# Performance work log

Measured on AMD Instinct MI355X. Metric: run time of the kernel, lower is better.

## Reference

```python
import jax, jax.numpy as jnp
import numpy as np

# Model constants (match init_kwargs)
IN_DIM = 1024   # input_dim == OLA frame size
ST_DIM = 128    # state_dim
HOP = IN_DIM // 2
N_FRAMES = 512
N_SAMPLES = 262144  # n_frames * hop
CTX = 512       # context_dim == control_plane_dim
HD = 32         # hypernetwork_dim
HL = 16         # hypernetwork_latent
B = 8


def _make_w(hv, A, Bm, i, o):
    # HyperNetworkLayer: hypervector -> latent -> flattened (i, o) matrix per batch
    return (hv @ A @ Bm).reshape(-1, i, o)


def setup_inputs() -> dict:
    key = jax.random.key(0)
    ks = jax.random.split(key, 17)
    s = 0.05
    return {
        'control_signal': jax.random.normal(ks[0], (B, CTX, N_FRAMES), jnp.float32),
        'state_hv': jax.random.normal(ks[1], (B, HD), jnp.float32),
        'output_hv': jax.random.normal(ks[2], (B, HD), jnp.float32),
        'input_hv': jax.random.normal(ks[3], (B, HD), jnp.float32),
        'direct_hv': jax.random.normal(ks[4], (B, HD), jnp.float32),
        'proj_hv': jax.random.normal(ks[5], (B, HD), jnp.float32),
        'times': jax.random.normal(ks[6], (B, 1, N_FRAMES), jnp.float32),
        # hypernetwork parameters (learned)
        'A_proj': jax.random.normal(ks[7], (HD, HL), jnp.float32) * s,
        'B_proj': jax.random.normal(ks[8], (HL, CTX * IN_DIM), jnp.float32) * s,
        'A_state': jax.random.normal(ks[9], (HD, HL), jnp.float32) * s,
        'B_state': jax.random.normal(ks[10], (HL, ST_DIM * ST_DIM), jnp.float32) * s,
        'A_input': jax.random.normal(ks[11], (HD, HL), jnp.float32) * s,
        'B_input': jax.random.normal(ks[12], (HL, IN_DIM * ST_DIM), jnp.float32) * s,
        'A_output': jax.random.normal(ks[13], (HD, HL), jnp.float32) * s,
        'B_output': jax.random.normal(ks[14], (HL, ST_DIM * IN_DIM), jnp.float32) * s,
        'A_direct': jax.random.normal(ks[15], (HD, HL), jnp.float32) * s,
        'B_direct': jax.random.normal(ks[16], (HL, IN_DIM * IN_DIM), jnp.float32) * s,
    }


def _forward(control_signal, state_hv, output_hv, input_hv, direct_hv, proj_hv, times,
             A_proj, B_proj, A_state, B_state, A_input, B_input,
             A_output, B_output, A_direct, B_direct):
    batch = control_signal.shape[0]
    dt = control_signal.dtype
    # per-batch hypernetwork-generated dense matrices
    Wp = _make_w(proj_hv, A_proj, B_proj, CTX, IN_DIM)       # [b, ctx, in]
    Ws = _make_w(state_hv, A_state, B_state, ST_DIM, ST_DIM)  # [b, st, st]
    Wi = _make_w(input_hv, A_input, B_input, IN_DIM, ST_DIM)  # [b, in, st]
    Wo = _make_w(output_hv, A_output, B_output, ST_DIM, IN_DIM)
    Wd = _make_w(direct_hv, A_direct, B_direct, IN_DIM, IN_DIM)

    ctrl = jnp.transpose(control_signal ** 2, (0, 2, 1))       # [b, fr, ctx]
    proj = jnp.einsum('bfc,bci->bfi', ctrl, Wp)                # [b, fr, in]

    def step(s, u):
        # s_i = A s_{i-1} + B u_i ; y_i = C (A s_{i-1}) + D u_i
        s2 = jnp.einsum('bs,bst->bt', s, Ws)
        y = jnp.einsum('bt,bti->bi', s2, Wo) + jnp.einsum('bi,bij->bj', u, Wd)
        s_new = s2 + jnp.einsum('bi,bis->bs', u, Wi)
        return s_new, y

    s0 = jnp.zeros((batch, ST_DIM), dt)
    _, outs = jax.lax.scan(step, s0, jnp.transpose(proj, (1, 0, 2)))  # [fr, b, in]
    outs = jnp.transpose(outs, (1, 0, 2))                              # [b, fr, in]

    # overlap-add with periodic hann window, hop = in_dim // 2
    win = 0.5 - 0.5 * jnp.cos(2.0 * jnp.pi * jnp.arange(IN_DIM, dtype=dt) / IN_DIM)
    windowed = outs * win
    total = HOP * (N_FRAMES - 1) + IN_DIM
    idx = jnp.arange(N_FRAMES)[:, None] * HOP + jnp.arange(IN_DIM)[None, :]  # [fr, in]
    buf = jnp.zeros((batch, total), dt).at[:, idx].add(windowed)
    sig = buf[:, :N_SAMPLES][:, None, :]   # [b, 1, n_samples]

    # DiracScheduler.schedule: softmax impulses over frames, upsample, FFT convolve
    impulses = jax.nn.softmax(times, axis=-1)                  # [b, 1, fr]
    up = jnp.zeros((batch, 1, N_SAMPLES), dt).at[:, :, ::N_SAMPLES // N_FRAMES].set(impulses)
    n = 2 * N_SAMPLES
    y = jnp.fft.irfft(jnp.fft.rfft(sig, n=n) * jnp.fft.rfft(up, n=n), n=n)[..., :N_SAMPLES]
    return y.astype(dt)


def reference(control_signal, state_hv, output_hv, input_hv, direct_hv, proj_hv, times,
              A_proj, B_proj, A_state, B_state, A_input, B_input,
              A_output, B_output, A_direct, B_direct):
    return _forward(control_signal, state_hv, output_hv, input_hv, direct_hv, proj_hv, times,
                    A_proj, B_proj, A_state, B_state, A_input, B_input,
                    A_output, B_output, A_direct, B_direct)
```

## Files before the change

kernel.cpp:

```cpp
#include <hip/hip_runtime.h>
#include <math.h>


typedef __attribute__((ext_vector_type(8))) short bfrag;
typedef __attribute__((ext_vector_type(4))) float f32x4;

__device__ inline unsigned short f2bf(float f) {
  unsigned int u = __float_as_uint(f);
  unsigned int r = (u + 0x7fff + ((u >> 16) & 1)) >> 16;
  return (unsigned short)r;
}

static const size_t OFF_LAT   = 0;
static const size_t OFF_IMP   = 1024;
static const size_t OFF_WPT   = 139264;
static const size_t OFF_WOT   = 2236416;
static const size_t OFF_WDIT  = 2760704;
static const size_t OFF_CTRLT = 7479296;
static const size_t OFF_PROJ  = 8527872;
static const size_t OFF_PROJD = 10625024;
static const size_t OFF_S2    = 15343616;
static const size_t OFF_MPOW  = 15605760;
static const size_t OFF_EC    = 16785408;
static const size_t OFF_HC    = 16850944;
static const size_t OFF_Y     = 16916480;
static const size_t OFF_SIG   = 21110784;
static const size_t OFF_T     = 23207936;

__global__ void latents_kernel(
    const float* __restrict__ hv_p, const float* __restrict__ hv_s,
    const float* __restrict__ hv_i, const float* __restrict__ hv_o,
    const float* __restrict__ hv_d,
    const float* __restrict__ A_p, const float* __restrict__ A_s,
    const float* __restrict__ A_i, const float* __restrict__ A_o,
    const float* __restrict__ A_d,
    float* __restrict__ lat) {
  int tid = threadIdx.x;
  if (tid >= 640) return;
  int m = tid >> 7, b = (tid >> 4) & 7, l = tid & 15;
  const float* hv; const float* A;
  switch (m) {
    case 0: hv = hv_p; A = A_p; break;
    case 1: hv = hv_s; A = A_s; break;
    case 2: hv = hv_i; A = A_i; break;
    case 3: hv = hv_o; A = A_o; break;
    default: hv = hv_d; A = A_d; break;
  }
  float acc = 0.f;
  for (int h = 0; h < 32; ++h) acc = fmaf(hv[b * 32 + h], A[h * 16 + l], acc);
  lat[tid] = acc;
}

__global__ __launch_bounds__(256) void build_w_kernel(
    const float* __restrict__ lat,
    const float* __restrict__ Bm,
    float* __restrict__ out,
    int total, size_t bstride) {
  int e = (blockIdx.x * 256 + threadIdx.x) * 4;
  if (e >= total) return;
  float4 v[16];
#pragma unroll
  for (int l = 0; l < 16; ++l)
    v[l] = *(const float4*)(Bm + (size_t)l * total + e);
#pragma unroll 1
  for (int b = 0; b < 8; ++b) {
    float ax = 0.f, ay = 0.f, az = 0.f, aw = 0.f;
#pragma unroll
    for (int l = 0; l < 16; ++l) {
      float lv = lat[b * 16 + l];
      ax = fmaf(lv, v[l].x, ax);
      ay = fmaf(lv, v[l].y, ay);
      az = fmaf(lv, v[l].z, az);
      aw = fmaf(lv, v[l].w, aw);
    }
    *(float4*)(out + (size_t)b * bstride + e) = make_float4(ax, ay, az, aw);
  }
}

__global__ __launch_bounds__(256) void build_wt_kernel(
    const float* __restrict__ lat,
    const float* __restrict__ Bm,
    unsigned short* __restrict__ out,
    int R, int C, size_t bstride) {
  __shared__ float ls[128];
  __shared__ unsigned short tile[32][36];
  int tid = threadIdx.x;
  if (tid < 128) ls[tid] = lat[tid];
  int cc = tid & 31, rg = tid >> 5;
  int c = blockIdx.x * 32 + cc;
  int r0 = blockIdx.y * 32 + rg * 4;
  size_t RC = (size_t)R * C;
  float bm[16][4];
#pragma unroll
  for (int l = 0; l < 16; ++l) {
    const float* p = Bm + (size_t)l * RC + (size_t)r0 * C + c;
#pragma unroll
    for (int j = 0; j < 4; ++j) bm[l][j] = p[(size_t)j * C];
  }
  int wc = tid >> 3, wrq = tid & 7;
  __syncthreads();
#pragma unroll 1
  for (int b = 0; b < 8; ++b) {
    float a0 = 0.f, a1 = 0.f, a2 = 0.f, a3 = 0.f;
#pragma unroll
    for (int l = 0; l < 16; ++l) {
      float lv = ls[b * 16 + l];
      a0 = fmaf(lv, bm[l][0], a0);
      a1 = fmaf(lv, bm[l][1], a1);
      a2 = fmaf(lv, bm[l][2], a2);
      a3 = fmaf(lv, bm[l][3], a3);
    }
    __syncthreads();
    ushort2 p0, p1;
    p0.x = f2bf(a0); p0.y = f2bf(a1);
    p1.x = f2bf(a2); p1.y = f2bf(a3);
    *(ushort2*)&tile[cc][rg * 4] = p0;
    *(ushort2*)&tile[cc][rg * 4 + 2] = p1;
    __syncthreads();
    ushort4 v = *(const ushort4*)&tile[wc][wrq * 4];
    *(ushort4*)(out + (size_t)b * bstride +
                (size_t)(blockIdx.x * 32 + wc) * R + blockIdx.y * 32 + wrq * 4) = v;
  }
}

__global__ void transpose_sq_kernel(const float* __restrict__ in,
                                    unsigned short* __restrict__ out) {
  __shared__ float tile[32][33];
  int b = blockIdx.z;
  int c0 = blockIdx.x * 32, f0 = blockIdx.y * 32;
  int tx = threadIdx.x, ty = threadIdx.y;
  const float* inb = in + (size_t)b * 512 * 512;
  unsigned short* outb = out + (size_t)b * 512 * 512;
#pragma unroll
  for (int i = 0; i < 4; ++i) {
    float v = inb[(size_t)(c0 + ty + i * 8) * 512 + f0 + tx];
    tile[ty + i * 8][tx] = v * v;
  }
  __syncthreads();
#pragma unroll
  for (int i = 0; i < 4; ++i)
    outb[(size_t)(f0 + ty + i * 8) * 512 + c0 + tx] = f2bf(tile[tx][ty + i * 8]);
}

template <int EPI, int CD_BF16, int TRI>
__global__ __launch_bounds__(256) void mfma_gemm_kernel(
    const unsigned short* __restrict__ A,
    const unsigned short* __restrict__ BT,
    const float* __restrict__ D, int ldd,
    void* __restrict__ Cout,
    int M, int N, int K) {
  const int b = blockIdx.z;
  A  += (size_t)b * M * K;
  BT += (size_t)b * N * K;
  const int m0 = blockIdx.y * 128;
  const int n0 = blockIdx.x * 128;
  __shared__ __align__(16) unsigned short As[2][128][40];
  __shared__ __align__(16) unsigned short Bs[2][128][40];
  const int tid = threadIdx.x;
  const int lane = tid & 63, wave = tid >> 6;
  const int wr = (wave >> 1) * 64, wc = (wave & 1) * 64;
  const int l15 = lane & 15, g = lane >> 4;
  f32x4 acc[4][4];
#pragma unroll
  for (int i = 0; i < 4; ++i)
#pragma unroll
    for (int j = 0; j < 4; ++j)
#pragma unroll
      for (int r = 0; r < 4; ++r) acc[i][j][r] = 0.f;

  const int srow = tid >> 2, soct = tid & 3;
  const unsigned short* Ag = A + (size_t)(m0 + srow) * K + soct * 8;
  const unsigned short* Bg = BT + (size_t)(n0 + srow) * K + soct * 8;
  const size_t row64 = (size_t)64 * K;
  const int kend = TRI ? (m0 + 128) : K;
  const int nt = kend >> 5;

  bfrag av0 = *(const bfrag*)(Ag);
  bfrag av1 = *(const bfrag*)(Ag + row64);
  bfrag bv0 = *(const bfrag*)(Bg);
  bfrag bv1 = *(const bfrag*)(Bg + row64);

  int cur = 0;
#pragma unroll 1
  for (int t = 0; t < nt; ++t) {
    *(bfrag*)(&As[cur][srow][soct * 8]) = av0;
    *(bfrag*)(&As[cur][64 + srow][soct * 8]) = av1;
    *(bfrag*)(&Bs[cur][srow][soct * 8]) = bv0;
    *(bfrag*)(&Bs[cur][64 + srow][soct * 8]) = bv1;
    __syncthreads();
    if (t + 1 < nt) {
      const int k0 = (t + 1) << 5;
      av0 = *(const bfrag*)(Ag + k0);
      av1 = *(const bfrag*)(Ag + row64 + k0);
      bv0 = *(const bfrag*)(Bg + k0);
      bv1 = *(const bfrag*)(Bg + row64 + k0);
    }
    bfrag af[4], bf[4];
#pragma unroll
    for (int mi = 0; mi < 4; ++mi)
      af[mi] = *(const bfrag*)(&As[cur][wr + mi * 16 + l15][g * 8]);
#pragma unroll
    for (int nj = 0; nj < 4; ++nj)
      bf[nj] = *(const bfrag*)(&Bs[cur][wc + nj * 16 + l15][g * 8]);
#pragma unroll
    for (int mi = 0; mi < 4; ++mi)
#pragma unroll
      for (int nj = 0; nj < 4; ++nj)
        acc[mi][nj] = __builtin_amdgcn_mfma_f32_16x16x32_bf16(af[mi], bf[nj], acc[mi][nj], 0, 0, 0);
    cur ^= 1;
  }

  float* Cf = (float*)Cout + (size_t)b * M * N;
  unsigned short* Cb = (unsigned short*)Cout + (size_t)b * M * N;
  if (EPI) D += (size_t)b * M * ldd;
#pragma unroll
  for (int nj = 0; nj < 4; ++nj) {
    int n = n0 + wc + nj * 16 + l15;
    float win = 0.f;
    if (EPI) win = 0.5f - 0.5f * cosf(6.28318530717958647693f * (float)n / 1024.0f);
#pragma unroll
    for (int mi = 0; mi < 4; ++mi) {
      int mbase = m0 + wr + mi * 16 + 4 * g;
#pragma unroll
      for (int r = 0; r < 4; ++r) {
        int m = mbase + r;
        float v = acc[mi][nj][r];
        if (EPI) v = (v + D[(size_t)m * ldd + n]) * win;
        if (CD_BF16) Cb[(size_t)m * N + n] = f2bf(v);
        else         Cf[(size_t)m * N + n] = v;
      }
    }
  }
}

__global__ __launch_bounds__(256) void powers_kernel(float* __restrict__ Mpow, int half) {
  int z = blockIdx.x;
  int b = z / half, k = z - b * half + 1;
  const float* A = Mpow + ((size_t)b * 9 + k) * 16384;
  const float* Bm = Mpow + ((size_t)b * 9 + half) * 16384;
  float* C = Mpow + ((size_t)b * 9 + half + k) * 16384;
  __shared__ __align__(16) float As[16][132];
  __shared__ __align__(16) float Bs[16][132];
  int tid = threadIdx.x;
  int tx = tid & 15, ty = tid >> 4;
  float acc[8][8];
#pragma unroll
  for (int i = 0; i < 8; ++i)
#pragma unroll
    for (int j = 0; j < 8; ++j) acc[i][j] = 0.f;
  int ar = tid >> 1, ac = (tid & 1) * 8;
  int br = tid >> 4, bc = (tid & 15) * 8;
  for (int k0 = 0; k0 < 128; k0 += 16) {
    float4 a0 = *(const float4*)(A + (size_t)ar * 128 + k0 + ac);
    float4 a1 = *(const float4*)(A + (size_t)ar * 128 + k0 + ac + 4);
    float4 b0 = *(const float4*)(Bm + (size_t)(k0 + br) * 128 + bc);
    float4 b1 = *(const float4*)(Bm + (size_t)(k0 + br) * 128 + bc + 4);
    __syncthreads();
    As[ac + 0][ar] = a0.x; As[ac + 1][ar] = a0.y; As[ac + 2][ar] = a0.z; As[ac + 3][ar] = a0.w;
    As[ac + 4][ar] = a1.x; As[ac + 5][ar] = a1.y; As[ac + 6][ar] = a1.z; As[ac + 7][ar] = a1.w;
    *(float4*)(&Bs[br][bc]) = b0;
    *(float4*)(&Bs[br][bc + 4]) = b1;
    __syncthreads();
#pragma unroll
    for (int kk = 0; kk < 16; ++kk) {
      float4 av0 = *(const float4*)(&As[kk][ty * 8]);
      float4 av1 = *(const float4*)(&As[kk][ty * 8 + 4]);
      float4 bv0 = *(const float4*)(&Bs[kk][tx * 8]);
      float4 bv1 = *(const float4*)(&Bs[kk][tx * 8 + 4]);
      float aa[8] = {av0.x, av0.y, av0.z, av0.w, av1.x, av1.y, av1.z, av1.w};
      float bb[8] = {bv0.x, bv0.y, bv0.z, bv0.w, bv1.x, bv1.y, bv1.z, bv1.w};
#pragma unroll
      for (int i = 0; i < 8; ++i)
#pragma unroll
        for (int j = 0; j < 8; ++j) acc[i][j] = fmaf(aa[i], bb[j], acc[i][j]);
    }
  }
#pragma unroll
  for (int i = 0; i < 8; ++i) {
    *(float4*)(C + (size_t)(ty * 8 + i) * 128 + tx * 8) =
        make_float4(acc[i][0], acc[i][1], acc[i][2], acc[i][3]);
    *(float4*)(C + (size_t)(ty * 8 + i) * 128 + tx * 8 + 4) =
        make_float4(acc[i][4], acc[i][5], acc[i][6], acc[i][7]);
  }
}

__global__ __launch_bounds__(256) void ec_kernel(
    const float* __restrict__ Mpow, const float* __restrict__ PD,
    float* __restrict__ Ec) {
  int b = blockIdx.x >> 6, c = blockIdx.x & 63;
  int tid = threadIdx.x, t = tid & 127, dh = tid >> 7;
  __shared__ __align__(16) float Bus[7][128];
  __shared__ float red[128];
  const float* Bu = PD + (size_t)b * 512 * 1152 + 1024;
  for (int idx = tid; idx < 896; idx += 256)
    Bus[idx >> 7][idx & 127] = Bu[(size_t)(c * 8 + (idx >> 7)) * 1152 + (idx & 127)];
  __syncthreads();
  float acc = 0.f;
  const float* Mb = Mpow + (size_t)b * 9 * 16384;
  int d0 = dh * 64;
#pragma unroll
  for (int i = 0; i < 7; ++i) {
    const float* Mk = Mb + (size_t)(7 - i) * 16384 + t;
#pragma unroll 8
    for (int d = 0; d < 64; ++d)
      acc = fmaf(Bus[i][d0 + d], Mk[(size_t)(d0 + d) * 128], acc);
  }
  if (dh == 1) red[t] = acc;
  __syncthreads();
  if (dh == 0) {
    float tot = acc + red[t] + Bu[(size_t)(c * 8 + 7) * 1152 + t];
    Ec[((size_t)b * 64 + c) * 128 + t] = tot;
  }
}

__global__ __launch_bounds__(128) void combine_kernel(
    const float* __restrict__ Mpow, const float* __restrict__ Ec,
    float* __restrict__ Hc) {
  int b = blockIdx.x, t = threadIdx.x;
  float w[128];
  const float* M8 = Mpow + ((size_t)b * 9 + 8) * 16384;
#pragma unroll
  for (int k = 0; k < 128; ++k) w[k] = M8[(size_t)k * 128 + t];
  __shared__ __align__(16) float ec_sh[64 * 128];
  const float* Ecb = Ec + (size_t)b * 8192;
#pragma unroll
  for (int i = 0; i < 16; ++i) {
    int idx = (t + i * 128) * 4;
    *(float4*)&ec_sh[idx] = *(const float4*)(Ecb + idx);
  }
  __shared__ __align__(16) float sh[2][128];
  sh[0][t] = 0.f;
  float* Hcb = Hc + (size_t)b * 8192;
  Hcb[t] = 0.f;
  __syncthreads();
  int cur = 0;
#pragma unroll 1
  for (int c = 0; c < 63; ++c) {
    float a0 = 0.f, a1 = 0.f, a2 = 0.f, a3 = 0.f;
#pragma unroll
    for (int k = 0; k < 128; k += 4) {
      float4 sv = *(const float4*)(&sh[cur][k]);
      a0 = fmaf(sv.x, w[k + 0], a0);
      a1 = fmaf(sv.y, w[k + 1], a1);
      a2 = fmaf(sv.z, w[k + 2], a2);
      a3 = fmaf(sv.w, w[k + 3], a3);
    }
    float hn = (a0 + a1) + (a2 + a3) + ec_sh[c * 128 + t];
    sh[cur ^ 1][t] = hn;
    Hcb[(c + 1) * 128 + t] = hn;
    __syncthreads();
    cur ^= 1;
  }
}

__global__ __launch_bounds__(256) void pass2_kernel(
    const float* __restrict__ Mpow, const float* __restrict__ PD,
    const float* __restrict__ Hc, unsigned short* __restrict__ S2) {
  int b = blockIdx.x >> 6, c = blockIdx.x & 63;
  int tid = threadIdx.x, t = tid & 127, dh = tid >> 7;
  __shared__ __align__(16) float Xs[15][128];
  __shared__ __align__(16) float red[8][128];
  const float* Bu = PD + (size_t)b * 512 * 1152 + 1024;
  for (int idx = tid; idx < 15 * 128; idx += 256) {
    int rr = idx >> 7, cc = idx & 127;
    float v = 0.f;
    if (rr == 7) v = Hc[((size_t)b * 64 + c) * 128 + cc];
    else if (rr > 7) v = Bu[(size_t)(c * 8 + rr - 8) * 1152 + cc];
    Xs[rr][cc] = v;
  }
  __syncthreads();
  float acc[8];
#pragma unroll
  for (int j = 0; j < 8; ++j) acc[j] = 0.f;
  const float* Mb = Mpow + (size_t)b * 9 * 16384;
  int d0 = dh * 64;
#pragma unroll 1
  for (int k = 1; k <= 8; ++k) {
    const float* Mk = Mb + (size_t)k * 16384 + t;
    const int xbase = 8 - k;
#pragma unroll 4
    for (int d4 = 0; d4 < 16; ++d4) {
      int d = d0 + d4 * 4;
      float m0 = Mk[(size_t)(d + 0) * 128];
      float m1 = Mk[(size_t)(d + 1) * 128];
      float m2 = Mk[(size_t)(d + 2) * 128];
      float m3 = Mk[(size_t)(d + 3) * 128];
#pragma unroll
      for (int j = 0; j < 8; ++j) {
        float4 xv = *(const float4*)(&Xs[xbase + j][d]);
        acc[j] = fmaf(xv.x, m0, acc[j]);
        acc[j] = fmaf(xv.y, m1, acc[j]);
        acc[j] = fmaf(xv.z, m2, acc[j]);
        acc[j] = fmaf(xv.w, m3, acc[j]);
      }
    }
  }
  if (dh == 1) {
#pragma unroll
    for (int j = 0; j < 8; ++j) red[j][t] = acc[j];
  }
  __syncthreads();
  if (dh == 0) {
    unsigned short* S2b = S2 + ((size_t)b * 512 + c * 8) * 128;
#pragma unroll
    for (int j = 0; j < 8; ++j)
      S2b[(size_t)j * 128 + t] = f2bf(acc[j] + red[j][t]);
  }
}

__global__ void softmax_kernel(const float* __restrict__ times, float* __restrict__ imp) {
  int b = blockIdx.x, t = threadIdx.x;
  __shared__ float red[512];
  float v = times[b * 512 + t];
  red[t] = v;
  __syncthreads();
  for (int s = 256; s > 0; s >>= 1) {
    if (t < s) red[t] = fmaxf(red[t], red[t + s]);
    __syncthreads();
  }
  float m = red[0];
  __syncthreads();
  float e = expf(v - m);
  red[t] = e;
  __syncthreads();
  for (int s = 256; s > 0; s >>= 1) {
    if (t < s) red[t] += red[t + s];
    __syncthreads();
  }
  imp[b * 512 + t] = e / red[0];
}

__global__ void toeplitz_kernel(const float* __restrict__ imp, unsigned short* __restrict__ T) {
  int idx = blockIdx.x * 256 + threadIdx.x;
  int b = idx >> 16;
  int rem = idx & 65535;
  int q = rem >> 7, p4 = (rem & 127) * 4;
  const float* impb = imp + b * 512;
  ushort4 o;
  o.x = (p4 + 0 <= q) ? f2bf(impb[q - p4 - 0]) : (unsigned short)0;
  o.y = (p4 + 1 <= q) ? f2bf(impb[q - p4 - 1]) : (unsigned short)0;
  o.z = (p4 + 2 <= q) ? f2bf(impb[q - p4 - 2]) : (unsigned short)0;
  o.w = (p4 + 3 <= q) ? f2bf(impb[q - p4 - 3]) : (unsigned short)0;
  *(ushort4*)(T + ((size_t)b * 512 + q) * 512 + p4) = o;
}

__global__ __launch_bounds__(256) void ola_transpose_kernel(const float* __restrict__ Y,
                                                            unsigned short* __restrict__ sigT) {
  __shared__ unsigned short tile[64][72];
  int b = blockIdx.z;
  int q0 = blockIdx.x * 64, r0 = blockIdx.y * 64;
  int tid = threadIdx.x;
  int rr = tid & 63, qg = tid >> 6;
  const float* Yb = Y + (size_t)b * 512 * 1024;
#pragma unroll
  for (int i = 0; i < 16; ++i) {
    int q = q0 + qg * 16 + i;
    float v = Yb[(size_t)q * 1024 + r0 + rr];
    if (q > 0) v += Yb[(size_t)(q - 1) * 1024 + 512 + r0 + rr];
    tile[qg * 16 + i][rr] = f2bf(v);
  }
  __syncthreads();
  int rw = tid >> 2, qo = tid & 3;
  unsigned short* orow = sigT + ((size_t)b * 512 + r0 + rw) * 512 + q0 + qo * 16;
  ushort4 w0, w1, w2, w3;
  w0.x = tile[qo * 16 + 0][rw];  w0.y = tile[qo * 16 + 1][rw];
  w0.z = tile[qo * 16 + 2][rw];  w0.w = tile[qo * 16 + 3][rw];
  w1.x = tile[qo * 16 + 4][rw];  w1.y = tile[qo * 16 + 5][rw];
  w1.z = tile[qo * 16 + 6][rw];  w1.w = tile[qo * 16 + 7][rw];
  w2.x = tile[qo * 16 + 8][rw];  w2.y = tile[qo * 16 + 9][rw];
  w2.z = tile[qo * 16 + 10][rw]; w2.w = tile[qo * 16 + 11][rw];
  w3.x = tile[qo * 16 + 12][rw]; w3.y = tile[qo * 16 + 13][rw];
  w3.z = tile[qo * 16 + 14][rw]; w3.w = tile[qo * 16 + 15][rw];
  *(ushort4*)(orow + 0)  = w0;
  *(ushort4*)(orow + 4)  = w1;
  *(ushort4*)(orow + 8)  = w2;
  *(ushort4*)(orow + 12) = w3;
}

extern "C" void kernel_launch(void* const* d_in, const int* in_sizes, int n_in,
                              void* d_out, int out_size, void* d_ws, size_t ws_size,
                              hipStream_t stream) {
  const float* control   = (const float*)d_in[0];
  const float* state_hv  = (const float*)d_in[1];
  const float* output_hv = (const float*)d_in[2];
  const float* input_hv  = (const float*)d_in[3];
  const float* direct_hv = (const float*)d_in[4];
  const float* proj_hv   = (const float*)d_in[5];
  const float* times     = (const float*)d_in[6];
  const float* A_proj   = (const float*)d_in[7];
  const float* B_proj   = (const float*)d_in[8];
  const float* A_state  = (const float*)d_in[9];
  const float* B_state  = (const float*)d_in[10];
  const float* A_input  = (const float*)d_in[11];
  const float* B_input  = (const float*)d_in[12];
  const float* A_output = (const float*)d_in[13];
  const float* B_output = (const float*)d_in[14];
  const float* A_direct = (const float*)d_in[15];
  const float* B_direct = (const float*)d_in[16];

  float* ws = (float*)d_ws;
  float* lat  = ws + OFF_LAT;
  float* impw = ws + OFF_IMP;
  unsigned short* WpT   = (unsigned short*)(ws + OFF_WPT);
  unsigned short* WoT   = (unsigned short*)(ws + OFF_WOT);
  unsigned short* WdiT  = (unsigned short*)(ws + OFF_WDIT);
  unsigned short* ctrlT = (unsigned short*)(ws + OFF_CTRLT);
  unsigned short* proj  = (unsigned short*)(ws + OFF_PROJ);
  float* projD = ws + OFF_PROJD;
  unsigned short* S2 = (unsigned short*)(ws + OFF_S2);
  float* Mpow = ws + OFF_MPOW;
  float* Ec   = ws + OFF_EC;
  float* Hc   = ws + OFF_HC;
  float* Y    = ws + OFF_Y;
  unsigned short* sigT = (unsigned short*)(ws + OFF_SIG);
  unsigned short* Tb   = (unsigned short*)(ws + OFF_T);
  float* out  = (float*)d_out;

  latents_kernel<<<1, 640, 0, stream>>>(proj_hv, state_hv, input_hv, output_hv, direct_hv,
                                        A_proj, A_state, A_input, A_output, A_direct, lat);

  build_w_kernel<<<16, 256, 0, stream>>>(lat + 1 * 128, B_state, Mpow + 16384, 16384, 147456);

  build_wt_kernel<<<dim3(32, 16), 256, 0, stream>>>(lat + 0 * 128, B_proj, WpT, 512, 1024, 524288);
  build_wt_kernel<<<dim3(32, 32), 256, 0, stream>>>(lat + 4 * 128, B_direct, WdiT, 1024, 1024, 1179648);
  build_wt_kernel<<<dim3(4, 32), 256, 0, stream>>>(lat + 2 * 128, B_input, WdiT + 1024 * 1024, 1024, 128, 1179648);
  build_wt_kernel<<<dim3(32, 4), 256, 0, stream>>>(lat + 3 * 128, B_output, WoT, 128, 1024, 131072);

  transpose_sq_kernel<<<dim3(16, 16, 8), dim3(32, 8), 0, stream>>>(control, ctrlT);

  mfma_gemm_kernel<0, 1, 0><<<dim3(8, 4, 8), 256, 0, stream>>>(
      ctrlT, WpT, nullptr, 0, proj, 512, 1024, 512);

  mfma_gemm_kernel<0, 0, 0><<<dim3(9, 4, 8), 256, 0, stream>>>(
      proj, WdiT, nullptr, 0, projD, 512, 1152, 1024);

  powers_kernel<<<8, 256, 0, stream>>>(Mpow, 1);
  powers_kernel<<<16, 256, 0, stream>>>(Mpow, 2);
  powers_kernel<<<32, 256, 0, stream>>>(Mpow, 4);
  ec_kernel<<<512, 256, 0, stream>>>(Mpow, projD, Ec);
  combine_kernel<<<8, 128, 0, stream>>>(Mpow, Ec, Hc);
  pass2_kernel<<<512, 256, 0, stream>>>(Mpow, projD, Hc, S2);

  mfma_gemm_kernel<1, 0, 0><<<dim3(8, 4, 8), 256, 0, stream>>>(
      S2, WoT, projD, 1152, Y, 512, 1024, 128);

  softmax_kernel<<<8, 512, 0, stream>>>(times, impw);
  toeplitz_kernel<<<2048, 256, 0, stream>>>(impw, Tb);

  ola_transpose_kernel<<<dim3(8, 8, 8), 256, 0, stream>>>(Y, sigT);

  mfma_gemm_kernel<0, 0, 1><<<dim3(4, 4, 8), 256, 0, stream>>>(
      Tb, sigT, nullptr, 0, out, 512, 512, 512);
}
```

Before: 272.4 us.

## Merge weight-build kernels, fuse softmax/Toeplitz into conv GEMM, emit transposed bf16 Y

Replaces the latents, build_w, four build_wt and transpose launches with one megabuild kernel that computes latents per block and dispatches by block index. The softmax and Toeplitz construction are folded into a dedicated convolution MFMA kernel that builds the A tiles from shared-memory impulses, so the Toeplitz matrix is never written to global memory. The output GEMM now writes Y transposed in bf16, which lets a simple elementwise OLA kernel replace the shared-memory transpose. This cuts launch count and global traffic. In exchange, the softmax is recomputed in every conv block, the latent computation is repeated in every build block, and the intermediate Y is kept at lower precision.

Result: faster. 240.2 us (-11.8%).

```diff
diff --git a/kernel.cpp b/kernel.cpp
--- a/kernel.cpp
+++ b/kernel.cpp
@@ -10,8 +10,10 @@
   unsigned int r = (u + 0x7fff + ((u >> 16) & 1)) >> 16;
   return (unsigned short)r;
 }
-
-static const size_t OFF_LAT   = 0;
+__device__ inline float bf2f(unsigned short u) {
+  return __uint_as_float(((unsigned int)u) << 16);
+}
+
 static const size_t OFF_IMP   = 1024;
 static const size_t OFF_WPT   = 139264;
 static const size_t OFF_WOT   = 2236416;
@@ -25,70 +27,89 @@
 static const size_t OFF_HC    = 16850944;
 static const size_t OFF_Y     = 16916480;
 static const size_t OFF_SIG   = 21110784;
-static const size_t OFF_T     = 23207936;
-
-__global__ void latents_kernel(
+
+__global__ __launch_bounds__(256) void megabuild_kernel(
     const float* __restrict__ hv_p, const float* __restrict__ hv_s,
     const float* __restrict__ hv_i, const float* __restrict__ hv_o,
     const float* __restrict__ hv_d,
     const float* __restrict__ A_p, const float* __restrict__ A_s,
     const float* __restrict__ A_i, const float* __restrict__ A_o,
     const float* __restrict__ A_d,
-    float* __restrict__ lat) {
-  int tid = threadIdx.x;
-  if (tid >= 640) return;
-  int m = tid >> 7, b = (tid >> 4) & 7, l = tid & 15;
-  const float* hv; const float* A;
-  switch (m) {
-    case 0: hv = hv_p; A = A_p; break;
-    case 1: hv = hv_s; A = A_s; break;
-    case 2: hv = hv_i; A = A_i; break;
-    case 3: hv = hv_o; A = A_o; break;
-    default: hv = hv_d; A = A_d; break;
-  }
-  float acc = 0.f;
-  for (int h = 0; h < 32; ++h) acc = fmaf(hv[b * 32 + h], A[h * 16 + l], acc);
-  lat[tid] = acc;
-}
-
-__global__ __launch_bounds__(256) void build_w_kernel(
-    const float* __restrict__ lat,
-    const float* __restrict__ Bm,
-    float* __restrict__ out,
-    int total, size_t bstride) {
-  int e = (blockIdx.x * 256 + threadIdx.x) * 4;
-  if (e >= total) return;
-  float4 v[16];
-#pragma unroll
-  for (int l = 0; l < 16; ++l)
-    v[l] = *(const float4*)(Bm + (size_t)l * total + e);
-#pragma unroll 1
-  for (int b = 0; b < 8; ++b) {
-    float ax = 0.f, ay = 0.f, az = 0.f, aw = 0.f;
-#pragma unroll
-    for (int l = 0; l < 16; ++l) {
-      float lv = lat[b * 16 + l];
-      ax = fmaf(lv, v[l].x, ax);
-      ay = fmaf(lv, v[l].y, ay);
-      az = fmaf(lv, v[l].z, az);
-      aw = fmaf(lv, v[l].w, aw);
-    }
-    *(float4*)(out + (size_t)b * bstride + e) = make_float4(ax, ay, az, aw);
-  }
-}
-
-__global__ __launch_bounds__(256) void build_wt_kernel(
-    const float* __restrict__ lat,
-    const float* __restrict__ Bm,
-    unsigned short* __restrict__ out,
-    int R, int C, size_t bstride) {
+    const float* __restrict__ B_p, const float* __restrict__ B_s,
+    const float* __restrict__ B_i, const float* __restrict__ B_o,
+    const float* __restrict__ B_d,
+    const float* __restrict__ control,
+    unsigned short* __restrict__ WpT, unsigned short* __restrict__ WoT,
+    unsigned short* __restrict__ WdiT, float* __restrict__ Ws1,
+    unsigned short* __restrict__ ctrlT) {
   __shared__ float ls[128];
   __shared__ unsigned short tile[32][36];
-  int tid = threadIdx.x;
-  if (tid < 128) ls[tid] = lat[tid];
+  __shared__ float ttile[32][33];
+  const int blk = blockIdx.x;
+  const int tid = threadIdx.x;
+
+  if (blk >= 1808) {
+    int z = blk - 1808;
+    int b = z >> 8;
+    int c0 = (z & 15) * 32, f0 = ((z >> 4) & 15) * 32;
+    int tx = tid & 31, ty = tid >> 5;
+    const float* inb = control + (size_t)b * 512 * 512;
+    unsigned short* outb = ctrlT + (size_t)b * 512 * 512;
+#pragma unroll
+    for (int i = 0; i < 4; ++i) {
+      float v = inb[(size_t)(c0 + ty + i * 8) * 512 + f0 + tx];
+      ttile[ty + i * 8][tx] = v * v;
+    }
+    __syncthreads();
+#pragma unroll
+    for (int i = 0; i < 4; ++i)
+      outb[(size_t)(f0 + ty + i * 8) * 512 + c0 + tx] = f2bf(ttile[tx][ty + i * 8]);
+    return;
+  }
+
+  const float* hv; const float* Am; const float* Bm;
+  unsigned short* outw = nullptr; int R = 0, C = 0; size_t bstride = 0; int bx = 0, by = 0;
+  int role;
+  if (blk < 512)        { role = 0; hv = hv_p; Am = A_p; Bm = B_p; outw = WpT;  R = 512;  C = 1024; bstride = 524288;  bx = blk & 31;           by = blk >> 5; }
+  else if (blk < 1536)  { role = 1; hv = hv_d; Am = A_d; Bm = B_d; outw = WdiT; R = 1024; C = 1024; bstride = 1179648; bx = (blk - 512) & 31;   by = (blk - 512) >> 5; }
+  else if (blk < 1664)  { role = 2; hv = hv_i; Am = A_i; Bm = B_i; outw = WdiT + 1024 * 1024; R = 1024; C = 128; bstride = 1179648; bx = (blk - 1536) & 3; by = (blk - 1536) >> 2; }
+  else if (blk < 1792)  { role = 3; hv = hv_o; Am = A_o; Bm = B_o; outw = WoT;  R = 128;  C = 1024; bstride = 131072;  bx = (blk - 1664) & 31;  by = (blk - 1664) >> 5; }
+  else                  { role = 4; hv = hv_s; Am = A_s; Bm = B_s; }
+
+  if (tid < 128) {
+    int b = tid >> 4, l = tid & 15;
+    float acc = 0.f;
+#pragma unroll
+    for (int h = 0; h < 32; ++h) acc = fmaf(hv[b * 32 + h], Am[h * 16 + l], acc);
+    ls[tid] = acc;
+  }
+  __syncthreads();
+
+  if (role == 4) {
+    int e = ((blk - 1792) * 256 + tid) * 4;
+    float4 v[16];
+#pragma unroll
+    for (int l = 0; l < 16; ++l)
+      v[l] = *(const float4*)(Bm + (size_t)l * 16384 + e);
+#pragma unroll 1
+    for (int b = 0; b < 8; ++b) {
+      float ax = 0.f, ay = 0.f, az = 0.f, aw = 0.f;
+#pragma unroll
+      for (int l = 0; l < 16; ++l) {
+        float lv = ls[b * 16 + l];
+        ax = fmaf(lv, v[l].x, ax);
+        ay = fmaf(lv, v[l].y, ay);
+        az = fmaf(lv, v[l].z, az);
+        aw = fmaf(lv, v[l].w, aw);
+      }
+      *(float4*)(Ws1 + (size_t)b * 147456 + e) = make_float4(ax, ay, az, aw);
+    }
+    return;
+  }
+
   int cc = tid & 31, rg = tid >> 5;
-  int c = blockIdx.x * 32 + cc;
-  int r0 = blockIdx.y * 32 + rg * 4;
+  int c = bx * 32 + cc;
+  int r0 = by * 32 + rg * 4;
   size_t RC = (size_t)R * C;
   float bm[16][4];
 #pragma unroll
@@ -98,7 +119,6 @@
     for (int j = 0; j < 4; ++j) bm[l][j] = p[(size_t)j * C];
   }
   int wc = tid >> 3, wrq = tid & 7;
-  __syncthreads();
 #pragma unroll 1
   for (int b = 0; b < 8; ++b) {
     float a0 = 0.f, a1 = 0.f, a2 = 0.f, a3 = 0.f;
@@ -118,31 +138,12 @@
     *(ushort2*)&tile[cc][rg * 4 + 2] = p1;
     __syncthreads();
     ushort4 v = *(const ushort4*)&tile[wc][wrq * 4];
-    *(ushort4*)(out + (size_t)b * bstride +
-                (size_t)(blockIdx.x * 32 + wc) * R + blockIdx.y * 32 + wrq * 4) = v;
-  }
-}
-
-__global__ void transpose_sq_kernel(const float* __restrict__ in,
-                                    unsigned short* __restrict__ out) {
-  __shared__ float tile[32][33];
-  int b = blockIdx.z;
-  int c0 = blockIdx.x * 32, f0 = blockIdx.y * 32;
-  int tx = threadIdx.x, ty = threadIdx.y;
-  const float* inb = in + (size_t)b * 512 * 512;
-  unsigned short* outb = out + (size_t)b * 512 * 512;
-#pragma unroll
-  for (int i = 0; i < 4; ++i) {
-    float v = inb[(size_t)(c0 + ty + i * 8) * 512 + f0 + tx];
-    tile[ty + i * 8][tx] = v * v;
-  }
-  __syncthreads();
-#pragma unroll
-  for (int i = 0; i < 4; ++i)
-    outb[(size_t)(f0 + ty + i * 8) * 512 + c0 + tx] = f2bf(tile[tx][ty + i * 8]);
-}
-
-template <int EPI, int CD_BF16, int TRI>
+    *(ushort4*)(outw + (size_t)b * bstride +
+                (size_t)(bx * 32 + wc) * R + by * 32 + wrq * 4) = v;
+  }
+}
+
+template <int EPI, int OUTM>
 __global__ __launch_bounds__(256) void mfma_gemm_kernel(
     const unsigned short* __restrict__ A,
     const unsigned short* __restrict__ BT,
@@ -172,8 +173,7 @@
   const unsigned short* Ag = A + (size_t)(m0 + srow) * K + soct * 8;
   const unsigned short* Bg = BT + (size_t)(n0 + srow) * K + soct * 8;
   const size_t row64 = (size_t)64 * K;
-  const int kend = TRI ? (m0 + 128) : K;
-  const int nt = kend >> 5;
+  const int nt = K >> 5;
 
   bfrag av0 = *(const bfrag*)(Ag);
   bfrag av1 = *(const bfrag*)(Ag + row64);
@@ -221,13 +221,22 @@
 #pragma unroll
     for (int mi = 0; mi < 4; ++mi) {
       int mbase = m0 + wr + mi * 16 + 4 * g;
+      float v[4];
 #pragma unroll
       for (int r = 0; r < 4; ++r) {
-        int m = mbase + r;
-        float v = acc[mi][nj][r];
-        if (EPI) v = (v + D[(size_t)m * ldd + n]) * win;
-        if (CD_BF16) Cb[(size_t)m * N + n] = f2bf(v);
-        else         Cf[(size_t)m * N + n] = v;
+        v[r] = acc[mi][nj][r];
+        if (EPI) v[r] = (v[r] + D[(size_t)(mbase + r) * ldd + n]) * win;
+      }
+      if (OUTM == 2) {
+        ushort4 o;
+        o.x = f2bf(v[0]); o.y = f2bf(v[1]); o.z = f2bf(v[2]); o.w = f2bf(v[3]);
+        *(ushort4*)(Cb + (size_t)n * M + mbase) = o;
+      } else {
+#pragma unroll
+        for (int r = 0; r < 4; ++r) {
+          if (OUTM == 1) Cb[(size_t)(mbase + r) * N + n] = f2bf(v[r]);
+          else           Cf[(size_t)(mbase + r) * N + n] = v[r];
+        }
       }
     }
   }
@@ -408,73 +417,127 @@
   }
 }
 
-__global__ void softmax_kernel(const float* __restrict__ times, float* __restrict__ imp) {
-  int b = blockIdx.x, t = threadIdx.x;
-  __shared__ float red[512];
-  float v = times[b * 512 + t];
-  red[t] = v;
-  __syncthreads();
-  for (int s = 256; s > 0; s >>= 1) {
-    if (t < s) red[t] = fmaxf(red[t], red[t + s]);
-    __syncthreads();
-  }
-  float m = red[0];
-  __syncthreads();
-  float e = expf(v - m);
-  red[t] = e;
-  __syncthreads();
-  for (int s = 256; s > 0; s >>= 1) {
-    if (t < s) red[t] += red[t + s];
-    __syncthreads();
-  }
-  imp[b * 512 + t] = e / red[0];
-}
-
-__global__ void toeplitz_kernel(const float* __restrict__ imp, unsigned short* __restrict__ T) {
+__global__ void ola_kernel(const unsigned short* __restrict__ YT,
+                           unsigned short* __restrict__ sigT) {
   int idx = blockIdx.x * 256 + threadIdx.x;
   int b = idx >> 16;
   int rem = idx & 65535;
-  int q = rem >> 7, p4 = (rem & 127) * 4;
-  const float* impb = imp + b * 512;
+  int r = rem >> 7, p4 = (rem & 127) * 4;
+  const unsigned short* Y1 = YT + (size_t)b * 524288 + (size_t)r * 512 + p4;
+  const unsigned short* Y2 = YT + (size_t)b * 524288 + (size_t)(512 + r) * 512 + p4 - 1;
+  ushort4 t1 = *(const ushort4*)Y1;
+  float o0 = bf2f(t1.x), o1 = bf2f(t1.y), o2 = bf2f(t1.z), o3 = bf2f(t1.w);
+  if (p4 > 0) o0 += bf2f(Y2[0]);
+  o1 += bf2f(Y2[1]);
+  o2 += bf2f(Y2[2]);
+  o3 += bf2f(Y2[3]);
   ushort4 o;
-  o.x = (p4 + 0 <= q) ? f2bf(impb[q - p4 - 0]) : (unsigned short)0;
-  o.y = (p4 + 1 <= q) ? f2bf(impb[q - p4 - 1]) : (unsigned short)0;
-  o.z = (p4 + 2 <= q) ? f2bf(impb[q - p4 - 2]) : (unsigned short)0;
-  o.w = (p4 + 3 <= q) ? f2bf(impb[q - p4 - 3]) : (unsigned short)0;
-  *(ushort4*)(T + ((size_t)b * 512 + q) * 512 + p4) = o;
-}
-
-__global__ __launch_bounds__(256) void ola_transpose_kernel(const float* __restrict__ Y,
-                                                            unsigned short* __restrict__ sigT) {
-  __shared__ unsigned short tile[64][72];
-  int b = blockIdx.z;
-  int q0 = blockIdx.x * 64, r0 = blockIdx.y * 64;
-  int tid = threadIdx.x;
-  int rr = tid & 63, qg = tid >> 6;
-  const float* Yb = Y + (size_t)b * 512 * 1024;
-#pragma unroll
-  for (int i = 0; i < 16; ++i) {
-    int q = q0 + qg * 16 + i;
-    float v = Yb[(size_t)q * 1024 + r0 + rr];
-    if (q > 0) v += Yb[(size_t)(q - 1) * 1024 + 512 + r0 + rr];
-    tile[qg * 16 + i][rr] = f2bf(v);
-  }
-  __syncthreads();
-  int rw = tid >> 2, qo = tid & 3;
-  unsigned short* orow = sigT + ((size_t)b * 512 + r0 + rw) * 512 + q0 + qo * 16;
-  ushort4 w0, w1, w2, w3;
-  w0.x = tile[qo * 16 + 0][rw];  w0.y = tile[qo * 16 + 1][rw];
-  w0.z = tile[qo * 16 + 2][rw];  w0.w = tile[qo * 16 + 3][rw];
-  w1.x = tile[qo * 16 + 4][rw];  w1.y = tile[qo * 16 + 5][rw];
-  w1.z = tile[qo * 16 + 6][rw];  w1.w = tile[qo * 16 + 7][rw];
-  w2.x = tile[qo * 16 + 8][rw];  w2.y = tile[qo * 16 + 9][rw];
-  w2.z = tile[qo * 16 + 10][rw]; w2.w = tile[qo * 16 + 11][rw];
-  w3.x = tile[qo * 16 + 12][rw]; w3.y = tile[qo * 16 + 13][rw];
-  w3.z = tile[qo * 16 + 14][rw]; w3.w = tile[qo * 16 + 15][rw];
-  *(ushort4*)(orow + 0)  = w0;
-  *(ushort4*)(orow + 4)  = w1;
-  *(ushort4*)(orow + 8)  = w2;
-  *(ushort4*)(orow + 12) = w3;
+  o.x = f2bf(o0); o.y = f2bf(o1); o.z = f2bf(o2); o.w = f2bf(o3);
+  *(ushort4*)(sigT + (size_t)b * 262144 + (size_t)r * 512 + p4) = o;
+}
+
+__global__ __launch_bounds__(256) void conv_mfma_kernel(
+    const float* __restrict__ times,
+    const unsigned short* __restrict__ sigT,
+    float* __restrict__ out) {
+  const int b = blockIdx.z;
+  const int m0 = blockIdx.y * 128;
+  const int n0 = blockIdx.x * 128;
+  __shared__ unsigned short imp_bf[512];
+  __shared__ float red[256];
+  __shared__ __align__(16) unsigned short As[2][128][40];
+  __shared__ __align__(16) unsigned short Bs[2][128][40];
+  const int tid = threadIdx.x;
+
+  float v0 = times[b * 512 + tid], v1 = times[b * 512 + 256 + tid];
+  red[tid] = fmaxf(v0, v1);
+  __syncthreads();
+  for (int s = 128; s > 0; s >>= 1) {
+    if (tid < s) red[tid] = fmaxf(red[tid], red[tid + s]);
+    __syncthreads();
+  }
+  float mx = red[0];
+  __syncthreads();
+  float e0 = expf(v0 - mx), e1 = expf(v1 - mx);
+  red[tid] = e0 + e1;
+  __syncthreads();
+  for (int s = 128; s > 0; s >>= 1) {
+    if (tid < s) red[tid] += red[tid + s];
+    __syncthreads();
+  }
+  float inv = 1.f / red[0];
+  imp_bf[tid] = f2bf(e0 * inv);
+  imp_bf[256 + tid] = f2bf(e1 * inv);
+  __syncthreads();
+
+  const int lane = tid & 63, wave = tid >> 6;
+  const int wr = (wave >> 1) * 64, wc = (wave & 1) * 64;
+  const int l15 = lane & 15, g = lane >> 4;
+  f32x4 acc[4][4];
+#pragma unroll
+  for (int i = 0; i < 4; ++i)
+#pragma unroll
+    for (int j = 0; j < 4; ++j)
+#pragma unroll
+      for (int r = 0; r < 4; ++r) acc[i][j][r] = 0.f;
+
+  const int srow = tid >> 2, soct = tid & 3;
+  const int q0 = m0 + srow, q1 = m0 + 64 + srow;
+  const unsigned short* Bg = sigT + (size_t)b * 262144 + (size_t)(n0 + srow) * 512 + soct * 8;
+  const size_t row64 = (size_t)64 * 512;
+  const int nt = (m0 + 128) >> 5;
+
+  bfrag bv0 = *(const bfrag*)(Bg);
+  bfrag bv1 = *(const bfrag*)(Bg + row64);
+
+  int cur = 0;
+#pragma unroll 1
+  for (int t = 0; t < nt; ++t) {
+    const int k0 = t << 5;
+    bfrag av0, av1;
+#pragma unroll
+    for (int j = 0; j < 8; ++j) {
+      int p = k0 + soct * 8 + j;
+      av0[j] = (p <= q0) ? (short)imp_bf[q0 - p] : (short)0;
+      av1[j] = (p <= q1) ? (short)imp_bf[q1 - p] : (short)0;
+    }
+    *(bfrag*)(&As[cur][srow][soct * 8]) = av0;
+    *(bfrag*)(&As[cur][64 + srow][soct * 8]) = av1;
+    *(bfrag*)(&Bs[cur][srow][soct * 8]) = bv0;
+    *(bfrag*)(&Bs[cur][64 + srow][soct * 8]) = bv1;
+    __syncthreads();
+    if (t + 1 < nt) {
+      const int kn = (t + 1) << 5;
+      bv0 = *(const bfrag*)(Bg + kn);
+      bv1 = *(const bfrag*)(Bg + row64 + kn);
+    }
+    bfrag af[4], bf[4];
+#pragma unroll
+    for (int mi = 0; mi < 4; ++mi)
+      af[mi] = *(const bfrag*)(&As[cur][wr + mi * 16 + l15][g * 8]);
+#pragma unroll
+    for (int nj = 0; nj < 4; ++nj)
+      bf[nj] = *(const bfrag*)(&Bs[cur][wc + nj * 16 + l15][g * 8]);
+#pragma unroll
+    for (int mi = 0; mi < 4; ++mi)
+#pragma unroll
+      for (int nj = 0; nj < 4; ++nj)
+        acc[mi][nj] = __builtin_amdgcn_mfma_f32_16x16x32_bf16(af[mi], bf[nj], acc[mi][nj], 0, 0, 0);
+    cur ^= 1;
+  }
+
+  float* Cf = out + (size_t)b * 262144;
+#pragma unroll
+  for (int nj = 0; nj < 4; ++nj) {
+    int n = n0 + wc + nj * 16 + l15;
+#pragma unroll
+    for (int mi = 0; mi < 4; ++mi) {
+      int mbase = m0 + wr + mi * 16 + 4 * g;
+#pragma unroll
+      for (int r = 0; r < 4; ++r)
+        Cf[(size_t)(mbase + r) * 512 + n] = acc[mi][nj][r];
+    }
+  }
 }
 
 extern "C" void kernel_launch(void* const* d_in, const int* in_sizes, int n_in,
@@ -499,8 +562,6 @@
   const float* B_direct = (const float*)d_in[16];
 
   float* ws = (float*)d_ws;
-  float* lat  = ws + OFF_LAT;
-  float* impw = ws + OFF_IMP;
   unsigned short* WpT   = (unsigned short*)(ws + OFF_WPT);
   unsigned short* WoT   = (unsigned short*)(ws + OFF_WOT);
   unsigned short* WdiT  = (unsigned short*)(ws + OFF_WDIT);
@@ -511,27 +572,20 @@
   float* Mpow = ws + OFF_MPOW;
   float* Ec   = ws + OFF_EC;
   float* Hc   = ws + OFF_HC;
-  float* Y    = ws + OFF_Y;
+  unsigned short* YT   = (unsigned short*)(ws + OFF_Y);
   unsigned short* sigT = (unsigned short*)(ws + OFF_SIG);
-  unsigned short* Tb   = (unsigned short*)(ws + OFF_T);
   float* out  = (float*)d_out;
 
-  latents_kernel<<<1, 640, 0, stream>>>(proj_hv, state_hv, input_hv, output_hv, direct_hv,
-                                        A_proj, A_state, A_input, A_output, A_direct, lat);
-
-  build_w_kernel<<<16, 256, 0, stream>>>(lat + 1 * 128, B_state, Mpow + 16384, 16384, 147456);
-
-  build_wt_kernel<<<dim3(32, 16), 256, 0, stream>>>(lat + 0 * 128, B_proj, WpT, 512, 1024, 524288);
-  build_wt_kernel<<<dim3(32, 32), 256, 0, stream>>>(lat + 4 * 128, B_direct, WdiT, 1024, 1024, 1179648);
-  build_wt_kernel<<<dim3(4, 32), 256, 0, stream>>>(lat + 2 * 128, B_input, WdiT + 1024 * 1024, 1024, 128, 1179648);
-  build_wt_kernel<<<dim3(32, 4), 256, 0, stream>>>(lat + 3 * 128, B_output, WoT, 128, 1024, 131072);
-
-  transpose_sq_kernel<<<dim3(16, 16, 8), dim3(32, 8), 0, stream>>>(control, ctrlT);
-
-  mfma_gemm_kernel<0, 1, 0><<<dim3(8, 4, 8), 256, 0, stream>>>(
+  megabuild_kernel<<<3856, 256, 0, stream>>>(
+      proj_hv, state_hv, input_hv, output_hv, direct_hv,
+      A_proj, A_state, A_input, A_output, A_direct,
+      B_proj, B_state, B_input, B_output, B_direct,
+      control, WpT, WoT, WdiT, Mpow + 16384, ctrlT);
+
+  mfma_gemm_kernel<0, 1><<<dim3(8, 4, 8), 256, 0, stream>>>(
       ctrlT, WpT, nullptr, 0, proj, 512, 1024, 512);
 
-  mfma_gemm_kernel<0, 0, 0><<<dim3(9, 4, 8), 256, 0, stream>>>(
+  mfma_gemm_kernel<0, 0><<<dim3(9, 4, 8), 256, 0, stream>>>(
       proj, WdiT, nullptr, 0, projD, 512, 1152, 1024);
 
   powers_kernel<<<8, 256, 0, stream>>>(Mpow, 1);
@@ -541,14 +595,10 @@
   combine_kernel<<<8, 128, 0, stream>>>(Mpow, Ec, Hc);
   pass2_kernel<<<512, 256, 0, stream>>>(Mpow, projD, Hc, S2);
 
-  mfma_gemm_kernel<1, 0, 0><<<dim3(8, 4, 8), 256, 0, stream>>>(
-      S2, WoT, projD, 1152, Y, 512, 1024, 128);
-
-  softmax_kernel<<<8, 512, 0, stream>>>(times, impw);
-  toeplitz_kernel<<<2048, 256, 0, stream>>>(impw, Tb);
-
-  ola_transpose_kernel<<<dim3(8, 8, 8), 256, 0, stream>>>(Y, sigT);
-
-  mfma_gemm_kernel<0, 0, 1><<<dim3(4, 4, 8), 256, 0, stream>>>(
-      Tb, sigT, nullptr, 0, out, 512, 512, 512);
-}
+  mfma_gemm_kernel<1, 2><<<dim3(8, 4, 8), 256, 0, stream>>>(
+      S2, WoT, projD, 1152, YT, 512, 1024, 128);
+
+  ola_kernel<<<2048, 256, 0, stream>>>(YT, sigT);
+
+  conv_mfma_kernel<<<dim3(4, 4, 8), 256, 0, stream>>>(times, sigT, out);
+}
```
